# Performance work log

Measured on AMD Instinct MI355X. Metric: run time of the kernel, lower is better.

## Reference

```python
import jax, jax.numpy as jnp
import numpy as np

# Model dims (mamba_ssm defaults: expand=2, d_state=16, d_conv=4, dt_rank=ceil(d_model/16))
V, D_MODEL, N_LAYERS = 32000, 768, 2
D_INNER, D_STATE, D_CONV, DT_RANK = 1536, 16, 4, 48
BATCH, SEQ = 2, 2048


def setup_inputs() -> dict:
    key = jax.random.key(0)
    ks = jax.random.split(key, 10)

    def nrm(k, shape, s=0.02):
        return (jax.random.normal(k, shape) * s).astype(jnp.float32)

    x = jax.random.randint(ks[0], (BATCH, SEQ), 0, V)
    emb = nrm(ks[1], (V, D_MODEL))
    # per-layer Mamba params, stacked on leading layer axis
    W_in = nrm(ks[2], (N_LAYERS, 2 * D_INNER, D_MODEL))          # in_proj (no bias)
    conv_w = nrm(ks[3], (N_LAYERS, D_INNER, 1, D_CONV), 0.1)      # depthwise causal conv
    conv_b = jnp.zeros((N_LAYERS, D_INNER), jnp.float32)
    W_x = nrm(ks[4], (N_LAYERS, DT_RANK + 2 * D_STATE, D_INNER))  # x_proj (no bias)
    W_dt = nrm(ks[5], (N_LAYERS, D_INNER, DT_RANK), 0.05)         # dt_proj
    b_dt = jnp.full((N_LAYERS, D_INNER), -4.0, jnp.float32)       # softplus(-4) ~ small dt
    # A initialized as -exp(A_log) with A_log = log(1..d_state), per mamba_ssm
    A_log = jnp.log(jnp.broadcast_to(
        jnp.arange(1, D_STATE + 1, dtype=jnp.float32), (N_LAYERS, D_INNER, D_STATE)))
    D_skip = jnp.ones((N_LAYERS, D_INNER), jnp.float32)
    W_out = nrm(ks[6], (N_LAYERS, D_MODEL, D_INNER))              # out_proj (no bias)
    ln_g = jnp.ones((D_MODEL,), jnp.float32)
    ln_b = jnp.zeros((D_MODEL,), jnp.float32)
    head_w = nrm(ks[7], (V, D_MODEL))
    head_b = jnp.zeros((V,), jnp.float32)
    return dict(x=x, emb=emb, W_in=W_in, conv_w=conv_w, conv_b=conv_b, W_x=W_x,
                W_dt=W_dt, b_dt=b_dt, A_log=A_log, D_skip=D_skip, W_out=W_out,
                ln_g=ln_g, ln_b=ln_b, head_w=head_w, head_b=head_b)


def mamba_block(h, W_in, conv_w, conv_b, W_x, W_dt, b_dt, A_log, D_skip, W_out):
    # h: (B, L, D_MODEL)
    xz = jnp.einsum('bld,ed->ble', h, W_in)              # (B, L, 2*d_inner)
    u, z = jnp.split(xz, 2, axis=-1)
    # causal depthwise conv over time
    uc = jnp.transpose(u, (0, 2, 1))                     # (B, d_inner, L)
    uc = jax.lax.conv_general_dilated(
        uc, conv_w, window_strides=(1,), padding=[(D_CONV - 1, 0)],
        feature_group_count=D_INNER, dimension_numbers=('NCH', 'OIH', 'NCH'))
    u = jax.nn.silu(jnp.transpose(uc, (0, 2, 1)) + conv_b)
    # input-dependent dt, B, C
    x_dbl = jnp.einsum('bld,ed->ble', u, W_x)            # (B, L, dt_rank+2*d_state)
    dtl, Bm, Cm = jnp.split(x_dbl, [DT_RANK, DT_RANK + D_STATE], axis=-1)
    dt = jax.nn.softplus(jnp.einsum('blr,dr->bld', dtl, W_dt) + b_dt)  # (B, L, d_inner)
    A = -jnp.exp(A_log)                                  # (d_inner, d_state)

    def step(hst, inp):
        dt_t, u_t, B_t, C_t = inp                        # (B,d_inner),(B,d_inner),(B,d_state),(B,d_state)
        hst = jnp.exp(dt_t[..., None] * A) * hst + (dt_t * u_t)[..., None] * B_t[:, None, :]
        y_t = jnp.einsum('bds,bs->bd', hst, C_t)
        return hst, y_t

    h0 = jnp.zeros((u.shape[0], D_INNER, D_STATE), u.dtype)
    xs = (dt.transpose(1, 0, 2), u.transpose(1, 0, 2),
          Bm.transpose(1, 0, 2), Cm.transpose(1, 0, 2))
    _, ys = jax.lax.scan(step, h0, xs)                   # (L, B, d_inner)
    y = ys.transpose(1, 0, 2) + u * D_skip
    y = y * jax.nn.silu(z)
    return jnp.einsum('bli,oi->blo', y, W_out)           # back to (B, L, D_MODEL)


def reference(x, emb, W_in, conv_w, conv_b, W_x, W_dt, b_dt, A_log, D_skip,
              W_out, ln_g, ln_b, head_w, head_b):
    h = emb[x]                                           # (B, L, D_MODEL)
    for l in range(N_LAYERS):
        h = h + mamba_block(h, W_in[l], conv_w[l], conv_b[l], W_x[l], W_dt[l],
                            b_dt[l], A_log[l], D_skip[l], W_out[l])
    mu = jnp.mean(h, axis=-1, keepdims=True)
    var = jnp.mean((h - mu) ** 2, axis=-1, keepdims=True)
    hn = (h - mu) * jax.lax.rsqrt(var + 1e-5) * ln_g + ln_b
    return jnp.einsum('bld,vd->blv', hn, head_w) + head_b
```

## Files before the change

kernel.cpp:

```cpp
#include <hip/hip_runtime.h>
#include <hip/hip_bf16.h>
#include <stdint.h>

#define BL    4096
#define DM    768
#define DI    1536
#define DS    16
#define DCONV 4
#define DTR   48
#define NL    2
#define SEQL  2048
#define BATCH 2
#define VOC   32000
#define NCH   32
#define CT    64

typedef __bf16 bf16_t;
typedef __bf16 bf16x8 __attribute__((ext_vector_type(8)));
typedef __bf16 bf16x4 __attribute__((ext_vector_type(4)));
typedef float  f32x4  __attribute__((ext_vector_type(4)));

__device__ __forceinline__ float sigmoidf_(float x) { return 1.f / (1.f + __expf(-x)); }

__global__ __launch_bounds__(256) void k_embed(const int* __restrict__ x,
                                               const float* __restrict__ emb,
                                               float* __restrict__ h,
                                               bf16_t* __restrict__ hb) {
  int row = blockIdx.x;
  int tok = x[row];
  const float* e = emb + (size_t)tok * DM;
  float* hr = h + (size_t)row * DM;
  bf16_t* hbr = hb + (size_t)row * DM;
  for (int c = threadIdx.x; c < DM; c += 256) {
    float v = e[c];
    hr[c] = v;
    hbr[c] = (bf16_t)v;
  }
}

__global__ __launch_bounds__(256) void k_cvt(const float* __restrict__ src,
                                             bf16_t* __restrict__ dst, long n4) {
  long i = (long)blockIdx.x * 256 + threadIdx.x;
  if (i >= n4) return;
  float4 v = ((const float4*)src)[i];
  bf16x4 o;
  o[0] = (bf16_t)v.x; o[1] = (bf16_t)v.y; o[2] = (bf16_t)v.z; o[3] = (bf16_t)v.w;
  ((bf16x4*)dst)[i] = o;
}

__global__ __launch_bounds__(256) void k_cvt_pad(const float* __restrict__ src,
                                                 bf16_t* __restrict__ dst,
                                                 int R, int C, int srcLd, int Cpad,
                                                 long total) {
  long i = (long)blockIdx.x * 256 + threadIdx.x;
  if (i >= total) return;
  int r = (int)(i / Cpad), c = (int)(i % Cpad);
  float v = (r < R && c < C) ? src[(size_t)r * srcLd + c] : 0.f;
  dst[i] = (bf16_t)v;
}

__global__ __launch_bounds__(256) void k_conv(const float* __restrict__ xz,
                                              const float* __restrict__ cw,
                                              const float* __restrict__ cb,
                                              float* __restrict__ uc,
                                              bf16_t* __restrict__ ucb, long total) {
  long i = (long)blockIdx.x * 256 + threadIdx.x;
  if (i >= total) return;
  int d = (int)(i % DI);
  long row = i / DI;
  int l = (int)(row % SEQL);
  const float* w = cw + (size_t)d * DCONV;
  float s = cb[d];
#pragma unroll
  for (int j = 0; j < DCONV; j++) {
    int lj = l - (DCONV - 1) + j;
    if (lj >= 0) s += xz[(row - (DCONV - 1) + j) * (2 * DI) + d] * w[j];
  }
  float v = s * sigmoidf_(s);
  uc[i] = v;
  ucb[i] = (bf16_t)v;
}

__global__ __launch_bounds__(256) void k_scan1(const float* __restrict__ dt,
                                               const float* __restrict__ uc,
                                               const float* __restrict__ xdbl,
                                               const float* __restrict__ A_log,
                                               float* __restrict__ cA,
                                               float* __restrict__ cB) {
  int gi = blockIdx.x * 256 + threadIdx.x;
  int s = gi & 15;
  int rest = gi >> 4;
  int d = rest % DI;
  int rest2 = rest / DI;
  int c = rest2 % NCH;
  int b = rest2 / NCH;
  float a = -__expf(A_log[d * DS + s]);
  long l0 = (long)c * CT;
  const float* dtp = dt + ((long)b * SEQL + l0) * DI + d;
  const float* ucp = uc + ((long)b * SEQL + l0) * DI + d;
  const float* Bp  = xdbl + ((long)b * SEQL + l0) * 80 + DTR + s;
  float S = 0.f, hh = 0.f;
#pragma unroll 4
  for (int l = 0; l < CT; l++) {
    float dtv = dtp[(long)l * DI];
    float uv  = ucp[(long)l * DI];
    float Bv  = Bp[(long)l * 80];
    S += dtv;
    hh = __expf(dtv * a) * hh + (dtv * uv) * Bv;
  }
  cA[gi] = __expf(a * S);
  cB[gi] = hh;
}

__global__ __launch_bounds__(256) void k_scan2(const float* __restrict__ cA,
                                               const float* __restrict__ cB,
                                               float* __restrict__ hst) {
  int gj = blockIdx.x * 256 + threadIdx.x;
  int ds_ = gj & (DI * DS - 1);
  int b = gj / (DI * DS);
  float h = 0.f;
#pragma unroll
  for (int c = 0; c < NCH; c++) {
    long idx = ((long)(b * NCH + c) * DI * DS) + ds_;
    hst[idx] = h;
    h = cA[idx] * h + cB[idx];
  }
}

__global__ __launch_bounds__(256) void k_scan3g(const float* __restrict__ dt,
                                                const float* __restrict__ uc,
                                                const float* __restrict__ xdbl,
                                                const float* __restrict__ A_log,
                                                const float* __restrict__ hst,
                                                const float* __restrict__ xz,
                                                const float* __restrict__ Dsk,
                                                bf16_t* __restrict__ o) {
  int gi = blockIdx.x * 256 + threadIdx.x;
  int s = gi & 15;
  int rest = gi >> 4;
  int d = rest % DI;
  int rest2 = rest / DI;
  int c = rest2 % NCH;
  int b = rest2 / NCH;
  float a = -__expf(A_log[d * DS + s]);
  float dval = Dsk[d];
  long l0 = (long)c * CT;
  const float* dtp = dt + ((long)b * SEQL + l0) * DI + d;
  const float* ucp = uc + ((long)b * SEQL + l0) * DI + d;
  const float* Bp  = xdbl + ((long)b * SEQL + l0) * 80 + DTR + s;
  const float* Cp  = Bp + DS;
  const float* zp  = xz + ((long)b * SEQL + l0) * (2 * DI) + DI + d;
  bf16_t* yp = o + ((long)b * SEQL + l0) * DI + d;
  float h = hst[gi];
#pragma unroll 4
  for (int l = 0; l < CT; l++) {
    float dtv = dtp[(long)l * DI];
    float uv  = ucp[(long)l * DI];
    float Bv  = Bp[(long)l * 80];
    float Cv  = Cp[(long)l * 80];
    h = __expf(dtv * a) * h + (dtv * uv) * Bv;
    float y = h * Cv;
    y += __shfl_xor(y, 1);
    y += __shfl_xor(y, 2);
    y += __shfl_xor(y, 4);
    y += __shfl_xor(y, 8);
    if (s == 0) {
      float z = zp[(long)l * 2 * DI];
      float yy = (y + uv * dval) * z * sigmoidf_(z);
      yp[(long)l * DI] = (bf16_t)yy;
    }
  }
}

__global__ __launch_bounds__(256) void k_ln(const float* __restrict__ h,
                                            const float* __restrict__ g,
                                            const float* __restrict__ bta,
                                            bf16_t* __restrict__ o) {
  __shared__ float sm[4];
  int row = blockIdx.x;
  int t = threadIdx.x;
  const float* hr = h + (long)row * DM;
  float v0 = hr[t], v1 = hr[t + 256], v2 = hr[t + 512];
  float s = v0 + v1 + v2;
#pragma unroll
  for (int off = 32; off > 0; off >>= 1) s += __shfl_down(s, off);
  if ((t & 63) == 0) sm[t >> 6] = s;
  __syncthreads();
  float mu = (sm[0] + sm[1] + sm[2] + sm[3]) * (1.f / DM);
  __syncthreads();
  float d0 = v0 - mu, d1 = v1 - mu, d2 = v2 - mu;
  float q = d0 * d0 + d1 * d1 + d2 * d2;
#pragma unroll
  for (int off = 32; off > 0; off >>= 1) q += __shfl_down(q, off);
  if ((t & 63) == 0) sm[t >> 6] = q;
  __syncthreads();
  float var = (sm[0] + sm[1] + sm[2] + sm[3]) * (1.f / DM);
  float rs = rsqrtf(var + 1e-5f);
  bf16_t* orow = o + (long)row * DM;
  orow[t]       = (bf16_t)(d0 * rs * g[t]       + bta[t]);
  orow[t + 256] = (bf16_t)(d1 * rs * g[t + 256] + bta[t + 256]);
  orow[t + 512] = (bf16_t)(d2 * rs * g[t + 512] + bta[t + 512]);
}

__device__ __forceinline__ void stage16(const bf16_t* gp, bf16_t* lp) {
  __builtin_amdgcn_global_load_lds(
      (const __attribute__((address_space(1))) uint32_t*)gp,
      (__attribute__((address_space(3))) uint32_t*)lp, 16, 0, 0);
}

template <int EPI>
__global__ __launch_bounds__(256) void k_gemm(const bf16_t* __restrict__ A,
                                              const bf16_t* __restrict__ W,
                                              float* __restrict__ C,
                                              const float* __restrict__ bias,
                                              bf16_t* __restrict__ side,
                                              int M, int N, int K, int ldc) {
  __shared__ bf16_t lA[128 * 32];
  __shared__ bf16_t lB[128 * 32];
  const int tid = threadIdx.x;
  const int lane = tid & 63;
  const int wv = tid >> 6;
  const int wm = wv >> 1, wn = wv & 1;
  const long m0 = (long)blockIdx.y * 128;
  const long n0 = (long)blockIdx.x * 128;
  const int r0 = tid >> 2;
  const int c8 = (tid & 3) * 8;
  const int fr = lane & 15;
  const int kq = lane >> 4;

  f32x4 acc[4][4];
#pragma unroll
  for (int i = 0; i < 4; i++)
#pragma unroll
    for (int j = 0; j < 4; j++) acc[i][j] = (f32x4){0.f, 0.f, 0.f, 0.f};

  const bf16_t* Ab = A + (m0 + r0) * (long)K + c8;
  const bf16_t* Wb = W + (n0 + r0) * (long)K + c8;
  bf16_t* lAp = lA + r0 * 32 + c8;
  bf16_t* lBp = lB + r0 * 32 + c8;
  const long s64K = 64L * K;

  for (int k0 = 0; k0 < K; k0 += 32) {
    __syncthreads();
    stage16(Ab + k0, lAp);
    stage16(Ab + k0 + s64K, lAp + 64 * 32);
    stage16(Wb + k0, lBp);
    stage16(Wb + k0 + s64K, lBp + 64 * 32);
    __syncthreads();
    bf16x8 af[4], bfv[4];
#pragma unroll
    for (int f = 0; f < 4; f++)
      af[f] = *(const bf16x8*)&lA[(wm * 64 + f * 16 + fr) * 32 + kq * 8];
#pragma unroll
    for (int f = 0; f < 4; f++)
      bfv[f] = *(const bf16x8*)&lB[(wn * 64 + f * 16 + fr) * 32 + kq * 8];
#pragma unroll
    for (int fm = 0; fm < 4; fm++)
#pragma unroll
      for (int fn = 0; fn < 4; fn++)
        acc[fm][fn] = __builtin_amdgcn_mfma_f32_16x16x32_bf16(af[fm], bfv[fn],
                                                              acc[fm][fn], 0, 0, 0);
  }

  const int r4 = (lane >> 4) * 4;
  const int cc = lane & 15;
#pragma unroll
  for (int fm = 0; fm < 4; fm++) {
    long rowb = m0 + wm * 64 + fm * 16 + r4;
#pragma unroll
    for (int fn = 0; fn < 4; fn++) {
      long col = n0 + wn * 64 + fn * 16 + cc;
      if (col < N) {
        float bv = (EPI == 3) ? bias[col] : 0.f;
#pragma unroll
        for (int r = 0; r < 4; r++) {
          long row = rowb + r;
          float v = acc[fm][fn][r];
          if (EPI == 3) { v += bv; v = (v > 20.f) ? v : log1pf(__expf(v)); }
          else if (EPI == 5) v += C[row * (long)ldc + col];
          C[row * (long)ldc + col] = v;
          if (EPI == 4 && col < 64)
            side[row * 64 + col] = (bf16_t)(col < DTR ? v : 0.f);
          if (EPI == 5)
            side[row * (long)ldc + col] = (bf16_t)v;
        }
      }
    }
  }
}


#define GLD256(ab, j, ktt, pp) do {                                             \
    int idx_ = (j) * 512 + tid;                                                 \
    int r_ = idx_ >> 3; int c16_ = idx_ & 7;                                    \
    size_t col_ = (size_t)(ktt) * 64 + (size_t)((c16_ ^ (r_ & 7)) << 3);        \
    const bf16_t* gp_ = (ab) ? (Wp + ((size_t)(n0 + r_)) * K + col_)            \
                             : (Ap + ((size_t)(m0 + r_)) * K + col_);           \
    bf16_t* lp_ = lds + ((((pp) * 2 + (ab)) * 256 + r_) * 64) + c16_ * 8;       \
    __builtin_amdgcn_global_load_lds(                                           \
        (const __attribute__((address_space(1))) uint32_t*)gp_,                 \
        (__attribute__((address_space(3))) uint32_t*)lp_, 16, 0, 0);            \
  } while (0)

#define STAGE2(pp, ktt, s) do {                                                 \
    if ((s) == 0) { GLD256(0, 0, ktt, pp); GLD256(0, 2, ktt, pp); }             \
    if ((s) == 1) { GLD256(1, 0, ktt, pp); GLD256(1, 1, ktt, pp); }             \
    if ((s) == 2) { GLD256(1, 2, ktt, pp); GLD256(1, 3, ktt, pp); }             \
    if ((s) == 3) { GLD256(0, 1, ktt, pp); GLD256(0, 3, ktt, pp); }             \
  } while (0)

#define COMPUTE256(pp, mg, kh) do {                                             \
    const char* lb_ = (const char*)lds;                                         \
    bf16x8 af_[4], bv_[4];                                                      \
    _Pragma("unroll") for (int f = 0; f < 4; ++f) {                             \
      int row_ = wm * 128 + (mg) * 64 + f * 16 + fr;                            \
      int byte_ = (((pp) * 2 + 0) * 256 + row_) * 128 +                         \
                  (((kh) * 64 + kq * 16) ^ ((row_ & 7) << 4));                  \
      af_[f] = *(const bf16x8*)(lb_ + byte_);                                   \
    }                                                                           \
    _Pragma("unroll") for (int f = 0; f < 4; ++f) {                             \
      int row_ = wn * 64 + f * 16 + fr;                                         \
      int byte_ = (((pp) * 2 + 1) * 256 + row_) * 128 +                         \
                  (((kh) * 64 + kq * 16) ^ ((row_ & 7) << 4));                  \
      bv_[f] = *(const bf16x8*)(lb_ + byte_);                                   \
    }                                                                           \
    __builtin_amdgcn_s_setprio(1);                                              \
    _Pragma("unroll") for (int fm = 0; fm < 4; ++fm)                            \
      _Pragma("unroll") for (int fn = 0; fn < 4; ++fn)                          \
        acc[(mg) * 4 + fm][fn] = __builtin_amdgcn_mfma_f32_16x16x32_bf16(       \
            af_[fm], bv_[fn], acc[(mg) * 4 + fm][fn], 0, 0, 0);                 \
    __builtin_amdgcn_s_setprio(0);                                              \
  } while (0)

#define WAITV2()  asm volatile("s_waitcnt vmcnt(2)" ::: "memory")
#define WAITV0()  asm volatile("s_waitcnt vmcnt(0)" ::: "memory")
#define BARRIER() do { __builtin_amdgcn_s_barrier();                            \
                       asm volatile("" ::: "memory"); } while (0)

template <int EPI>
__global__ __launch_bounds__(512, 2) void k_gemm256(const bf16_t* __restrict__ Ap,
                                                    const bf16_t* __restrict__ Wp,
                                                    float* __restrict__ C,
                                                    const float* __restrict__ bias,
                                                    int K, int ldc) {
  __shared__ bf16_t lds[2 * 2 * 256 * 64];
  const int tid = threadIdx.x;
  const int lane = tid & 63;
  const int wid = tid >> 6;
  const int wm = wid >> 2, wn = wid & 3;
  const int fr = lane & 15, kq = lane >> 4;

  const int cpx = gridDim.x >> 3;
  const int wg = ((int)blockIdx.x & 7) * cpx + ((int)blockIdx.x >> 3);
  const long m0 = (long)(wg & 15) * 256;
  const long n0 = (long)(wg >> 4) * 256;

  f32x4 acc[8][4];
#pragma unroll
  for (int i = 0; i < 8; i++)
#pragma unroll
    for (int j = 0; j < 4; j++) acc[i][j] = (f32x4){0.f, 0.f, 0.f, 0.f};

  STAGE2(0, 0, 0); STAGE2(0, 0, 1); STAGE2(0, 0, 2); STAGE2(0, 0, 3);
  WAITV2();
  BARRIER();

  const int NT = K >> 6;
  for (int kt = 0; kt < NT; ++kt) {
    const int p = kt & 1;
    const bool pre = (kt + 1 < NT);
    if (pre) STAGE2(p ^ 1, kt + 1, 0);
    COMPUTE256(p, 0, 0);
    if (pre) WAITV2(); else WAITV0();
    BARRIER();
    if (pre) STAGE2(p ^ 1, kt + 1, 1);
    COMPUTE256(p, 1, 0);
    if (pre) STAGE2(p ^ 1, kt + 1, 2);
    COMPUTE256(p, 0, 1);
    if (pre) STAGE2(p ^ 1, kt + 1, 3);
    COMPUTE256(p, 1, 1);
    if (pre) {
      WAITV2();
      BARRIER();
    }
  }

  const int r4 = (lane >> 4) * 4;
  const int cc = lane & 15;
#pragma unroll
  for (int m = 0; m < 8; m++) {
    long rowb = m0 + wm * 128 + (m >> 2) * 64 + (m & 3) * 16 + r4;
#pragma unroll
    for (int n = 0; n < 4; n++) {
      long col = n0 + wn * 64 + n * 16 + cc;
      float bv = (EPI == 1) ? bias[col] : 0.f;
#pragma unroll
      for (int r = 0; r < 4; r++) {
        float v = acc[m][n][r];
        if (EPI == 1) {
          v += bv;
          __builtin_nontemporal_store(v, &C[(rowb + r) * (long)ldc + col]);
        } else {
          C[(rowb + r) * (long)ldc + col] = v;
        }
      }
    }
  }
}

static inline int cdiv_l(long a, long b) { return (int)((a + b - 1) / b); }

extern "C" void kernel_launch(void* const* d_in, const int* in_sizes, int n_in,
                              void* d_out, int out_size, void* d_ws, size_t ws_size,
                              hipStream_t stream) {
  (void)in_sizes; (void)n_in; (void)out_size; (void)ws_size;
  const int*   x      = (const int*)  d_in[0];
  const float* emb    = (const float*)d_in[1];
  const float* W_in   = (const float*)d_in[2];
  const float* conv_w = (const float*)d_in[3];
  const float* conv_b = (const float*)d_in[4];
  const float* W_x    = (const float*)d_in[5];
  const float* W_dt   = (const float*)d_in[6];
  const float* b_dt   = (const float*)d_in[7];
  const float* A_log  = (const float*)d_in[8];
  const float* D_skip = (const float*)d_in[9];
  const float* W_out  = (const float*)d_in[10];
  const float* ln_g   = (const float*)d_in[11];
  const float* ln_b   = (const float*)d_in[12];
  const float* head_w = (const float*)d_in[13];
  const float* head_b = (const float*)d_in[14];
  float* out = (float*)d_out;

  char* ws = (char*)d_ws;
  bf16_t* abuf = (bf16_t*)ws;
  bf16_t* wbuf = (bf16_t*)(ws + (size_t)BL * DI * 2);

  float* xz   = out;
  float* uc   = xz   + (size_t)BL * 2 * DI;
  float* xdbl = uc   + (size_t)BL * DI;
  float* dtb  = xdbl + (size_t)BL * 80;
  float* ysb_unused = dtb + (size_t)BL * DI;  (void)ysb_unused;
  float* h    = dtb  + (size_t)BL * DI;
  float* cA   = h    + (size_t)BL * DM;
  float* cB   = cA   + (size_t)BATCH * NCH * DI * DS;
  float* hst  = cB   + (size_t)BATCH * NCH * DI * DS;
  bf16_t* hbf = (bf16_t*)(hst + (size_t)BATCH * DI * DS);
  bf16_t* dtl = hbf + (size_t)BL * DM;

  const int scan_blocks = BATCH * NCH * DI * DS / 256;
  const int st_blocks   = BATCH * DI * DS / 256;

  k_embed<<<BL, 256, 0, stream>>>(x, emb, h, hbf);

  for (int l = 0; l < NL; ++l) {
    k_cvt<<<cdiv_l((long)2 * DI * DM / 4, 256), 256, 0, stream>>>(
        W_in + (size_t)l * 2 * DI * DM, wbuf, (long)2 * DI * DM / 4);
    k_gemm256<0><<<(BL / 256) * (2 * DI / 256), 512, 0, stream>>>(
        hbf, wbuf, xz, nullptr, DM, 2 * DI);
    k_conv<<<cdiv_l((long)BL * DI, 256), 256, 0, stream>>>(
        xz, conv_w + (size_t)l * DI * DCONV, conv_b + (size_t)l * DI,
        uc, abuf, (long)BL * DI);
    k_cvt_pad<<<cdiv_l(128L * DI, 256), 256, 0, stream>>>(
        W_x + (size_t)l * 80 * DI, wbuf, 80, DI, DI, DI, 128L * DI);
    k_gemm<4><<<dim3(1, BL / 128), 256, 0, stream>>>(
        abuf, wbuf, xdbl, nullptr, dtl, BL, 80, DI, 80);
    k_cvt_pad<<<cdiv_l((long)DI * 64, 256), 256, 0, stream>>>(
        W_dt + (size_t)l * DI * DTR, wbuf, DI, DTR, DTR, 64, (long)DI * 64);
    k_gemm<3><<<dim3(DI / 128, BL / 128), 256, 0, stream>>>(
        dtl, wbuf, dtb, b_dt + (size_t)l * DI, nullptr, BL, DI, 64, DI);
    k_scan1<<<scan_blocks, 256, 0, stream>>>(dtb, uc, xdbl,
                                             A_log + (size_t)l * DI * DS, cA, cB);
    k_scan2<<<st_blocks, 256, 0, stream>>>(cA, cB, hst);
    k_scan3g<<<scan_blocks, 256, 0, stream>>>(dtb, uc, xdbl,
                                              A_log + (size_t)l * DI * DS, hst,
                                              xz, D_skip + (size_t)l * DI, abuf);
    k_cvt<<<cdiv_l((long)DM * DI / 4, 256), 256, 0, stream>>>(
        W_out + (size_t)l * DM * DI, wbuf, (long)DM * DI / 4);
    k_gemm<5><<<dim3(DM / 128, BL / 128), 256, 0, stream>>>(
        abuf, wbuf, h, nullptr, hbf, BL, DM, DI, DM);
  }

  k_ln<<<BL, 256, 0, stream>>>(h, ln_g, ln_b, abuf);
  k_cvt<<<cdiv_l((long)VOC * DM / 4, 256), 256, 0, stream>>>(head_w, wbuf, (long)VOC * DM / 4);
  k_gemm256<1><<<(BL / 256) * (VOC / 256), 512, 0, stream>>>(
      abuf, wbuf, out, head_b, DM, VOC);
}
```

Measured before the change: 1.110 ms.

## Batch weight conversions, split-K x_proj GEMM, and LDS-staged head epilogue

All weight fp32-to-bf16 conversions (in_proj, out_proj, head, x_proj, dt_proj) are merged into one launch at the start, with separate workspace buffers per layer, replacing the per-layer conversion launches. The x_proj GEMM, which previously ran on only 32 blocks, now uses a split-K kernel with atomic adds into a zeroed output, plus a separate pad kernel to build the dt low-rank input. The large GEMM epilogue is restaged through LDS so the logits are written with coalesced float4 nontemporal stores. Atomics make the x_proj sum order nondeterministic and add zeroing and pad launches.

```diff
diff --git a/kernel.cpp b/kernel.cpp
--- a/kernel.cpp
+++ b/kernel.cpp
@@ -38,14 +38,48 @@
   }
 }
 
-__global__ __launch_bounds__(256) void k_cvt(const float* __restrict__ src,
-                                             bf16_t* __restrict__ dst, long n4) {
+#define NV0 1179648L
+#define NV1 589824L
+#define NV2 6144000L
+#define NS3 393216L
+#define NS4 196608L
+#define NVT (NV0 + NV1 + NV2)
+#define NTOT (NVT + NS3 + NS4)
+
+__global__ __launch_bounds__(256) void k_cvtw(const float* __restrict__ Win,
+                                              const float* __restrict__ Wout,
+                                              const float* __restrict__ Whead,
+                                              const float* __restrict__ Wx,
+                                              const float* __restrict__ Wdt,
+                                              bf16_t* __restrict__ bin,
+                                              bf16_t* __restrict__ bout,
+                                              bf16_t* __restrict__ bhead,
+                                              bf16_t* __restrict__ bx,
+                                              bf16_t* __restrict__ bdt) {
   long i = (long)blockIdx.x * 256 + threadIdx.x;
-  if (i >= n4) return;
-  float4 v = ((const float4*)src)[i];
-  bf16x4 o;
-  o[0] = (bf16_t)v.x; o[1] = (bf16_t)v.y; o[2] = (bf16_t)v.z; o[3] = (bf16_t)v.w;
-  ((bf16x4*)dst)[i] = o;
+  if (i >= NTOT) return;
+  if (i < NVT) {
+    const float* s; bf16_t* d; long j = i;
+    if (i < NV0)            { s = Win;   d = bin; }
+    else if (i < NV0 + NV1) { s = Wout;  d = bout;  j = i - NV0; }
+    else                    { s = Whead; d = bhead; j = i - NV0 - NV1; }
+    float4 v = ((const float4*)s)[j];
+    bf16x4 o;
+    o[0] = (bf16_t)v.x; o[1] = (bf16_t)v.y; o[2] = (bf16_t)v.z; o[3] = (bf16_t)v.w;
+    ((bf16x4*)d)[j] = o;
+  } else if (i < NVT + NS3) {
+    long j = i - NVT;
+    int l = (int)(j / (128 * 1536));
+    int rr = (int)((j / 1536) % 128);
+    int c = (int)(j % 1536);
+    bx[j] = (bf16_t)(rr < 80 ? Wx[((long)l * 80 + rr) * 1536 + c] : 0.f);
+  } else {
+    long j = i - NVT - NS3;
+    int l = (int)(j / (1536 * 64));
+    int r = (int)((j / 64) % 1536);
+    int c = (int)(j & 63);
+    bdt[j] = (bf16_t)(c < DTR ? Wdt[((long)l * 1536 + r) * DTR + c] : 0.f);
+  }
 }
 
 __global__ __launch_bounds__(256) void k_cvt_pad(const float* __restrict__ src,
@@ -57,6 +91,11 @@
   int r = (int)(i / Cpad), c = (int)(i % Cpad);
   float v = (r < R && c < C) ? src[(size_t)r * srcLd + c] : 0.f;
   dst[i] = (bf16_t)v;
+}
+
+__global__ __launch_bounds__(256) void k_zero(float* __restrict__ p, long n4) {
+  long i = (long)blockIdx.x * 256 + threadIdx.x;
+  if (i < n4) ((float4*)p)[i] = (float4){0.f, 0.f, 0.f, 0.f};
 }
 
 __global__ __launch_bounds__(256) void k_conv(const float* __restrict__ xz,
@@ -279,11 +318,78 @@
           if (EPI == 3) { v += bv; v = (v > 20.f) ? v : log1pf(__expf(v)); }
           else if (EPI == 5) v += C[row * (long)ldc + col];
           C[row * (long)ldc + col] = v;
-          if (EPI == 4 && col < 64)
-            side[row * 64 + col] = (bf16_t)(col < DTR ? v : 0.f);
           if (EPI == 5)
             side[row * (long)ldc + col] = (bf16_t)v;
         }
+      }
+    }
+  }
+}
+
+__global__ __launch_bounds__(256) void k_gemm_sk(const bf16_t* __restrict__ A,
+                                                 const bf16_t* __restrict__ W,
+                                                 float* __restrict__ C,
+                                                 int N, int K, int KS, int ldc) {
+  __shared__ bf16_t lA[128 * 32];
+  __shared__ bf16_t lB[128 * 32];
+  const int tid = threadIdx.x;
+  const int lane = tid & 63;
+  const int wv = tid >> 6;
+  const int wm = wv >> 1, wn = wv & 1;
+  const long m0 = (long)blockIdx.y * 128;
+  const long n0 = (long)blockIdx.x * 128;
+  const int kLo = blockIdx.z * KS;
+  const int r0 = tid >> 2;
+  const int c8 = (tid & 3) * 8;
+  const int fr = lane & 15;
+  const int kq = lane >> 4;
+
+  f32x4 acc[4][4];
+#pragma unroll
+  for (int i = 0; i < 4; i++)
+#pragma unroll
+    for (int j = 0; j < 4; j++) acc[i][j] = (f32x4){0.f, 0.f, 0.f, 0.f};
+
+  const bf16_t* Ab = A + (m0 + r0) * (long)K + c8;
+  const bf16_t* Wb = W + (n0 + r0) * (long)K + c8;
+  bf16_t* lAp = lA + r0 * 32 + c8;
+  bf16_t* lBp = lB + r0 * 32 + c8;
+  const long s64K = 64L * K;
+
+  for (int k0 = kLo; k0 < kLo + KS; k0 += 32) {
+    __syncthreads();
+    stage16(Ab + k0, lAp);
+    stage16(Ab + k0 + s64K, lAp + 64 * 32);
+    stage16(Wb + k0, lBp);
+    stage16(Wb + k0 + s64K, lBp + 64 * 32);
+    __syncthreads();
+    bf16x8 af[4], bfv[4];
+#pragma unroll
+    for (int f = 0; f < 4; f++)
+      af[f] = *(const bf16x8*)&lA[(wm * 64 + f * 16 + fr) * 32 + kq * 8];
+#pragma unroll
+    for (int f = 0; f < 4; f++)
+      bfv[f] = *(const bf16x8*)&lB[(wn * 64 + f * 16 + fr) * 32 + kq * 8];
+#pragma unroll
+    for (int fm = 0; fm < 4; fm++)
+#pragma unroll
+      for (int fn = 0; fn < 4; fn++)
+        acc[fm][fn] = __builtin_amdgcn_mfma_f32_16x16x32_bf16(af[fm], bfv[fn],
+                                                              acc[fm][fn], 0, 0, 0);
+  }
+
+  const int r4 = (lane >> 4) * 4;
+  const int cc = lane & 15;
+#pragma unroll
+  for (int fm = 0; fm < 4; fm++) {
+    long rowb = m0 + wm * 64 + fm * 16 + r4;
+#pragma unroll
+    for (int fn = 0; fn < 4; fn++) {
+      long col = n0 + wn * 64 + fn * 16 + cc;
+      if (col < N) {
+#pragma unroll
+        for (int r = 0; r < 4; r++)
+          atomicAdd(&C[(rowb + r) * (long)ldc + col], acc[fm][fn][r]);
       }
     }
   }
@@ -385,23 +491,39 @@
     }
   }
 
-  const int r4 = (lane >> 4) * 4;
-  const int cc = lane & 15;
-#pragma unroll
-  for (int m = 0; m < 8; m++) {
-    long rowb = m0 + wm * 128 + (m >> 2) * 64 + (m & 3) * 16 + r4;
-#pragma unroll
-    for (int n = 0; n < 4; n++) {
-      long col = n0 + wn * 64 + n * 16 + cc;
-      float bv = (EPI == 1) ? bias[col] : 0.f;
-#pragma unroll
-      for (int r = 0; r < 4; r++) {
-        float v = acc[m][n][r];
+  {
+    float* lf = (float*)(void*)lds;
+    const int q = lane >> 4;
+    const int cc = lane & 15;
+    float4 bias4 = {0.f, 0.f, 0.f, 0.f};
+    if (EPI == 1) bias4 = *(const float4*)&bias[n0 + lane * 4];
+#pragma unroll
+    for (int p = 0; p < 4; ++p) {
+      __syncthreads();
+      if (wm == (p >> 1)) {
+        const int mgb = (p & 1) * 4;
+#pragma unroll
+        for (int m4 = 0; m4 < 4; ++m4)
+#pragma unroll
+          for (int n = 0; n < 4; ++n) {
+            f32x4 v = acc[mgb + m4][n];
+            float* dst = &lf[(m4 * 16 + q * 4) * 260 + wn * 64 + n * 16 + cc];
+#pragma unroll
+            for (int r = 0; r < 4; ++r) dst[r * 260] = v[r];
+          }
+      }
+      __syncthreads();
+      const long rowg0 = m0 + p * 64;
+#pragma unroll
+      for (int it = 0; it < 8; ++it) {
+        int row_loc = wid * 8 + it;
+        f32x4 v = *(const f32x4*)&lf[row_loc * 260 + lane * 4];
+        float* gp = &C[(rowg0 + row_loc) * (long)ldc + n0 + lane * 4];
         if (EPI == 1) {
-          v += bv;
-          __builtin_nontemporal_store(v, &C[(rowb + r) * (long)ldc + col]);
+          v[0] += bias4.x; v[1] += bias4.y; v[2] += bias4.z; v[3] += bias4.w;
+          __builtin_nontemporal_store(v, (f32x4*)gp);
         } else {
-          C[(rowb + r) * (long)ldc + col] = v;
+          *(f32x4*)gp = v;
         }
       }
     }
@@ -431,57 +553,56 @@
   const float* head_b = (const float*)d_in[14];
   float* out = (float*)d_out;
 
-  char* ws = (char*)d_ws;
-  bf16_t* abuf = (bf16_t*)ws;
-  bf16_t* wbuf = (bf16_t*)(ws + (size_t)BL * DI * 2);
+  bf16_t* abuf   = (bf16_t*)d_ws;
+  bf16_t* hbf    = abuf   + (size_t)BL * DI;
+  bf16_t* dtl    = hbf    + (size_t)BL * DM;
+  bf16_t* wb_in  = dtl    + (size_t)BL * 64;
+  bf16_t* wb_out = wb_in  + (size_t)2 * 3072 * 768;
+  bf16_t* wb_hd  = wb_out + (size_t)2 * 768 * 1536;
+  bf16_t* wb_x   = wb_hd  + (size_t)VOC * DM;
+  bf16_t* wb_dt  = wb_x   + (size_t)2 * 128 * 1536;
 
   float* xz   = out;
   float* uc   = xz   + (size_t)BL * 2 * DI;
   float* xdbl = uc   + (size_t)BL * DI;
   float* dtb  = xdbl + (size_t)BL * 80;
-  float* ysb_unused = dtb + (size_t)BL * DI;  (void)ysb_unused;
   float* h    = dtb  + (size_t)BL * DI;
   float* cA   = h    + (size_t)BL * DM;
   float* cB   = cA   + (size_t)BATCH * NCH * DI * DS;
   float* hst  = cB   + (size_t)BATCH * NCH * DI * DS;
-  bf16_t* hbf = (bf16_t*)(hst + (size_t)BATCH * DI * DS);
-  bf16_t* dtl = hbf + (size_t)BL * DM;
 
   const int scan_blocks = BATCH * NCH * DI * DS / 256;
   const int st_blocks   = BATCH * DI * DS / 256;
 
+  k_cvtw<<<cdiv_l(NTOT, 256), 256, 0, stream>>>(W_in, W_out, head_w, W_x, W_dt,
+                                                wb_in, wb_out, wb_hd, wb_x, wb_dt);
   k_embed<<<BL, 256, 0, stream>>>(x, emb, h, hbf);
 
   for (int l = 0; l < NL; ++l) {
-    k_cvt<<<cdiv_l((long)2 * DI * DM / 4, 256), 256, 0, stream>>>(
-        W_in + (size_t)l * 2 * DI * DM, wbuf, (long)2 * DI * DM / 4);
     k_gemm256<0><<<(BL / 256) * (2 * DI / 256), 512, 0, stream>>>(
-        hbf, wbuf, xz, nullptr, DM, 2 * DI);
+        hbf, wb_in + (size_t)l * 3072 * 768, xz, nullptr, DM, 2 * DI);
     k_conv<<<cdiv_l((long)BL * DI, 256), 256, 0, stream>>>(
         xz, conv_w + (size_t)l * DI * DCONV, conv_b + (size_t)l * DI,
         uc, abuf, (long)BL * DI);
-    k_cvt_pad<<<cdiv_l(128L * DI, 256), 256, 0, stream>>>(
-        W_x + (size_t)l * 80 * DI, wbuf, 80, DI, DI, DI, 128L * DI);
-    k_gemm<4><<<dim3(1, BL / 128), 256, 0, stream>>>(
-        abuf, wbuf, xdbl, nullptr, dtl, BL, 80, DI, 80);
-    k_cvt_pad<<<cdiv_l((long)DI * 64, 256), 256, 0, stream>>>(
-        W_dt + (size_t)l * DI * DTR, wbuf, DI, DTR, DTR, 64, (long)DI * 64);
+    k_zero<<<cdiv_l((long)BL * 80 / 4, 256), 256, 0, stream>>>(xdbl, (long)BL * 80 / 4);
+    k_gemm_sk<<<dim3(1, BL / 128, 4), 256, 0, stream>>>(
+        abuf, wb_x + (size_t)l * 128 * 1536, xdbl, 80, DI, DI / 4, 80);
+    k_cvt_pad<<<cdiv_l((long)BL * 64, 256), 256, 0, stream>>>(
+        xdbl, dtl, BL, DTR, 80, 64, (long)BL * 64);
     k_gemm<3><<<dim3(DI / 128, BL / 128), 256, 0, stream>>>(
-        dtl, wbuf, dtb, b_dt + (size_t)l * DI, nullptr, BL, DI, 64, DI);
+        dtl, wb_dt + (size_t)l * 1536 * 64, dtb, b_dt + (size_t)l * DI, nullptr,
+        BL, DI, 64, DI);
     k_scan1<<<scan_blocks, 256, 0, stream>>>(dtb, uc, xdbl,
                                              A_log + (size_t)l * DI * DS, cA, cB);
     k_scan2<<<st_blocks, 256, 0, stream>>>(cA, cB, hst);
     k_scan3g<<<scan_blocks, 256, 0, stream>>>(dtb, uc, xdbl,
                                               A_log + (size_t)l * DI * DS, hst,
                                               xz, D_skip + (size_t)l * DI, abuf);
-    k_cvt<<<cdiv_l((long)DM * DI / 4, 256), 256, 0, stream>>>(
-        W_out + (size_t)l * DM * DI, wbuf, (long)DM * DI / 4);
     k_gemm<5><<<dim3(DM / 128, BL / 128), 256, 0, stream>>>(
-        abuf, wbuf, h, nullptr, hbf, BL, DM, DI, DM);
+        abuf, wb_out + (size_t)l * 768 * 1536, h, nullptr, hbf, BL, DM, DI, DM);
   }
 
   k_ln<<<BL, 256, 0, stream>>>(h, ln_g, ln_b, abuf);
-  k_cvt<<<cdiv_l((long)VOC * DM / 4, 256), 256, 0, stream>>>(head_w, wbuf, (long)VOC * DM / 4);
   k_gemm256<1><<<(BL / 256) * (VOC / 256), 512, 0, stream>>>(
-      abuf, wbuf, out, head_b, DM, VOC);
-}
+      abuf, wb_hd, out, head_b, DM, VOC);
+}
```

New measurement: 1.056 ms. 4.9% less time.
